# Kernel tuning notes

Measured on AMD Instinct MI355X. Metric: run time of the kernel, lower is better.

## Reference

```python
import jax, jax.numpy as jnp
import numpy as np


def setup_inputs() -> dict:
    key = jax.random.key(0)
    kx, ky, kq, kk, kv = jax.random.split(key, 5)
    B, S, D = 4, 4096, 1024
    scale = 1.0 / np.sqrt(D)
    return {
        "X": jax.random.normal(kx, (B, S, D), dtype=jnp.float32),
        "Y": jax.random.normal(ky, (B, S, D), dtype=jnp.float32),
        "Wq": jax.random.normal(kq, (D, D), dtype=jnp.float32) * scale,
        "Wk": jax.random.normal(kk, (D, D), dtype=jnp.float32) * scale,
        "Wv": jax.random.normal(kv, (D, D), dtype=jnp.float32) * scale,
    }


def reference(X, Y, Wq, Wk, Wv):
    # Single-head windowed cross attention.
    # torch nn.Linear(y) == y @ W.T
    WINDOW = 256
    B, S, D = X.shape
    Q = jnp.einsum("bsd,ed->bse", Y, Wq)
    K = jnp.einsum("bsd,ed->bse", X, Wk)
    V = jnp.einsum("bsd,ed->bse", X, Wv)
    scores = jnp.einsum("bqd,bkd->bqk", Q, K) / jnp.sqrt(jnp.float32(D))
    i = jnp.arange(S)
    band = jnp.abs(i[:, None] - i[None, :]) <= WINDOW  # [S, S]
    NEG = jnp.float32(-1e10)  # matches torch masked_fill value
    scores = jnp.where(band[None, :, :], scores, NEG)
    attn = jax.nn.softmax(scores, axis=-1)
    return jnp.einsum("bqk,bkd->bqd", attn, V)
```

## Files before the change

kernel.cpp:

```cpp
#include <hip/hip_runtime.h>
#include <hip/hip_bf16.h>
#include <stdint.h>

typedef _Float16 half8 __attribute__((ext_vector_type(8)));
typedef float floatx4 __attribute__((ext_vector_type(4)));

#define MFMA16(a, b, c) __builtin_amdgcn_mfma_f32_16x16x32_f16(a, b, c, 0, 0, 0)

__device__ __forceinline__ void async_load16(const void* g, void* l) {
    __builtin_amdgcn_global_load_lds((__attribute__((address_space(1))) void*)(g),
                                     (__attribute__((address_space(3))) void*)(l),
                                     16, 0, 0);
}

#define RAW_BARRIER()  asm volatile("s_barrier" ::: "memory")
#define WAIT_VMCNT(n)  asm volatile("s_waitcnt vmcnt(" #n ")" ::: "memory")
#define WAIT_LGKM0()   asm volatile("s_waitcnt lgkmcnt(0)" ::: "memory")


__global__ __launch_bounds__(256) void cvt_kernel(const float* __restrict__ in,
                                                  _Float16* __restrict__ out,
                                                  int n, float scale) {
    int i = (blockIdx.x * 256 + threadIdx.x) * 8;
    if (i >= n) return;
    float4 v0 = *(const float4*)(in + i);
    float4 v1 = *(const float4*)(in + i + 4);
    half8 h;
    h[0] = (_Float16)(v0.x * scale);
    h[1] = (_Float16)(v0.y * scale);
    h[2] = (_Float16)(v0.z * scale);
    h[3] = (_Float16)(v0.w * scale);
    h[4] = (_Float16)(v1.x * scale);
    h[5] = (_Float16)(v1.y * scale);
    h[6] = (_Float16)(v1.z * scale);
    h[7] = (_Float16)(v1.w * scale);
    *(half8*)(out + i) = h;
}

__global__ __launch_bounds__(512, 2) void gemm_bt(const _Float16* __restrict__ A,
                                                  const _Float16* __restrict__ B,
                                                  _Float16* __restrict__ C,
                                                  int M, int N, int K) {
    __shared__ _Float16 sA[2][2][256 * 32];
    __shared__ _Float16 sB[2][2][256 * 32];
    const int tid  = threadIdx.x;
    const int lane = tid & 63;
    const int w    = tid >> 6;
    const int quad = lane >> 4;
    const int m16  = lane & 15;
    const int mq   = (w >> 2) * 64;
    const int nq   = (w & 3) * 32;

    const int gx = gridDim.x, gy = gridDim.y;
    const int total = gx * gy;
    const int id = blockIdx.y * gx + blockIdx.x;
    const int logical = (id & 7) * (total >> 3) + (id >> 3);
    int bx, by;
    if (gx <= gy) { bx = logical % gx; by = logical / gx; }
    else          { by = logical % gy; bx = logical / gy; }
    const long row0 = (long)by * 256;
    const long col0 = (long)bx * 256;

    floatx4 acc[8][4] = {};

    const int swz = ((tid & 3) ^ ((tid >> 3) & 3)) * 8;
    const _Float16* ga = A + (row0 + (tid >> 2)) * (long)K + swz;
    const _Float16* gb = B + (col0 + (tid >> 2)) * (long)K + swz;
    const int wchunk = w * 1024;

    auto stageA = [&](int tile, int half) {
        const int s = tile & 1;
        char* l0 = (char*)sA[s][0] + half * 8192 + wchunk;
        char* l1 = (char*)sA[s][1] + half * 8192 + wchunk;
        const _Float16* g = ga + (long)tile * 64 + (long)half * 128 * K;
        async_load16(g, l0);
        async_load16(g + 32, l1);
    };
    auto stageB = [&](int tile, int half) {
        const int s = tile & 1;
        char* l0 = (char*)sB[s][0] + half * 8192 + wchunk;
        char* l1 = (char*)sB[s][1] + half * 8192 + wchunk;
        const _Float16* g = gb + (long)tile * 64 + (long)half * 128 * K;
        async_load16(g, l0);
        async_load16(g + 32, l1);
    };

    const int rswz = (m16 >> 1) & 3;
    const int NTt  = K >> 6;

    stageA(0, 0); stageA(0, 1); stageB(0, 0); stageB(0, 1);
    stageA(1, 0); stageB(1, 0);
    WAIT_VMCNT(4);
    RAW_BARRIER();

    for (int U = 0; U < NTt; ++U) {
        const int s = U & 1;
        const int T1 = U + 1, T2 = U + 2;
        half8 af[4][2], bf[2][2];
#pragma unroll
        for (int p = 0; p < 4; ++p) {
            const int mh = p >> 1, nh = p & 1;
            if ((p & 1) == 0) {
#pragma unroll
                for (int mt = 0; mt < 4; mt++)
#pragma unroll
                    for (int j = 0; j < 2; j++)
                        af[mt][j] = *(const half8*)(sA[s][j] +
                            (mh * 128 + mq + mt * 16 + m16) * 32 + (quad ^ rswz) * 8);
            }
#pragma unroll
            for (int nt = 0; nt < 2; nt++)
#pragma unroll
                for (int j = 0; j < 2; j++)
                    bf[nt][j] = *(const half8*)(sB[s][j] +
                        (nh * 128 + nq + nt * 16 + m16) * 32 + (quad ^ rswz) * 8);
            if (p == 0 && T1 < NTt) stageB(T1, 1);
            if (p == 1 && T1 < NTt) stageA(T1, 1);
            if (p == 2 && T2 < NTt) stageA(T2, 0);
            if (p == 3 && T2 < NTt) stageB(T2, 0);
            if (p == 3) {
                if (T2 < NTt) { WAIT_VMCNT(4); }
                else          { WAIT_VMCNT(0); }
            }
            RAW_BARRIER();
            WAIT_LGKM0();
            __builtin_amdgcn_sched_barrier(0);
            __builtin_amdgcn_s_setprio(1);
#pragma unroll
            for (int mt = 0; mt < 4; mt++)
#pragma unroll
                for (int nt = 0; nt < 2; nt++) {
                    acc[mh * 4 + mt][nh * 2 + nt] =
                        MFMA16(af[mt][0], bf[nt][0], acc[mh * 4 + mt][nh * 2 + nt]);
                    acc[mh * 4 + mt][nh * 2 + nt] =
                        MFMA16(af[mt][1], bf[nt][1], acc[mh * 4 + mt][nh * 2 + nt]);
                }
            __builtin_amdgcn_s_setprio(0);
            RAW_BARRIER();
        }
    }

#pragma unroll
    for (int mt = 0; mt < 8; mt++)
#pragma unroll
        for (int nt = 0; nt < 4; nt++)
#pragma unroll
            for (int reg = 0; reg < 4; reg++) {
                long r = row0 + (mt >> 2) * 128 + mq + (mt & 3) * 16 + quad * 4 + reg;
                long c = col0 + (nt >> 1) * 128 + nq + (nt & 1) * 16 + m16;
                C[r * N + c] = (_Float16)acc[mt][nt][reg];
            }
}

__global__ __launch_bounds__(512) void qk_kernel(const _Float16* __restrict__ Qh,
                                                 const _Float16* __restrict__ Kh,
                                                 _Float16* __restrict__ Pg,
                                                 float* __restrict__ invSum) {
    const int S = 4096, D = 1024;
    __shared__ _Float16 sK[2][576 * 32];
    __shared__ _Float16 sQ[2][64 * 32];
    __shared__ float sMax[64][8];
    __shared__ float sSum[64][8];

    const int tid  = threadIdx.x;
    const int lane = tid & 63;
    const int w    = tid >> 6;
    const int quad = lane >> 4;
    const int c16  = lane & 15;
    const int qblk = (blockIdx.x & 7) * 32 + (blockIdx.x >> 3);
    const int b    = qblk >> 6;
    const int q0   = (qblk & 63) << 6;

    int kstart = q0 - 256; if (kstart < 0) kstart = 0;
    int kend   = q0 + 320; if (kend > S) kend = S;
    const int L = kend - kstart;
    const int ntiles = L >> 4;

    const int lrow = lane >> 2;
    const int swz  = ((lane & 3) ^ ((lane >> 3) & 3)) * 8;
    const _Float16* Kbase = Kh + ((long)(b * S + kstart) + lrow) * D + swz;
    const _Float16* Qbase = Qh + ((long)(b * S + q0) + w * 16 + lrow) * D + swz;

    auto stage = [&](int bi, int kc) {
#pragma unroll
        for (int j = 0; j < 5; j++) {
            int g = j * 8 + w;
            if (g < ntiles)
                async_load16(Kbase + (long)g * 16 * D + kc, (char*)sK[bi] + g * 1024);
        }
        if (w < 4)
            async_load16(Qbase + kc, (char*)sQ[bi] + w * 1024);
    };

    const int rswz = ((c16 >> 1) & 3);

    floatx4 acc[4][5] = {};
    stage(0, 0);
    for (int kc = 0; kc < 1024; kc += 32) {
        const int bi = (kc >> 5) & 1;
        __syncthreads();
        if (kc + 32 < 1024) stage(bi ^ 1, kc + 32);
        half8 aQ[4];
#pragma unroll
        for (int mt = 0; mt < 4; mt++)
            aQ[mt] = *(const half8*)(sQ[bi] + (mt * 16 + c16) * 32 + (quad ^ rswz) * 8);
#pragma unroll
        for (int i = 0; i < 5; i++) {
            int t = w + i * 8;
            if (t < ntiles) {
                half8 bK = *(const half8*)(sK[bi] + (t * 16 + c16) * 32 + (quad ^ rswz) * 8);
#pragma unroll
                for (int mt = 0; mt < 4; mt++)
                    acc[mt][i] = MFMA16(aQ[mt], bK, acc[mt][i]);
            }
        }
    }

#pragma unroll
    for (int i = 0; i < 5; i++) {
        int t = w + i * 8;
        if (t < ntiles) {
            int j = kstart + t * 16 + c16;
#pragma unroll
            for (int mt = 0; mt < 4; mt++)
#pragma unroll
                for (int r = 0; r < 4; r++) {
                    int qi = q0 + mt * 16 + quad * 4 + r;
                    int dd = qi - j; dd = dd < 0 ? -dd : dd;
                    if (dd > 256) acc[mt][i][r] = -1e30f;
                }
        }
    }
#pragma unroll
    for (int mt = 0; mt < 4; mt++)
#pragma unroll
        for (int r = 0; r < 4; r++) {
            float m = -1e30f;
#pragma unroll
            for (int i = 0; i < 5; i++)
                if (w + i * 8 < ntiles) m = fmaxf(m, acc[mt][i][r]);
#pragma unroll
            for (int off = 1; off < 16; off <<= 1) m = fmaxf(m, __shfl_xor(m, off, 64));
            if (c16 == 0) sMax[mt * 16 + quad * 4 + r][w] = m;
        }
    __syncthreads();
    if (tid < 64) {
        float fm = sMax[tid][0];
#pragma unroll
        for (int j = 1; j < 8; j++) fm = fmaxf(fm, sMax[tid][j]);
        sMax[tid][0] = fm;
    }
    __syncthreads();
#pragma unroll
    for (int mt = 0; mt < 4; mt++)
#pragma unroll
        for (int r = 0; r < 4; r++) {
            int row = mt * 16 + quad * 4 + r;
            float fm = sMax[row][0];
            float s = 0.f;
#pragma unroll
            for (int i = 0; i < 5; i++) {
                int t = w + i * 8;
                if (t < ntiles) {
                    float e = __expf(acc[mt][i][r] - fm);
                    s += e;
                    Pg[(long)qblk * 36864 + row * 576 + t * 16 + c16] = (_Float16)e;
                }
            }
#pragma unroll
            for (int off = 1; off < 16; off <<= 1) s += __shfl_xor(s, off, 64);
            if (c16 == 0) sSum[row][w] = s;
        }
    __syncthreads();
    if (tid < 64) {
        float t = 0.f;
#pragma unroll
        for (int j = 0; j < 8; j++) t += sSum[tid][j];
        invSum[qblk * 64 + tid] = 1.f / t;
    }
}

__global__ __launch_bounds__(512) void pv_kernel(const _Float16* __restrict__ Pg,
                                                 const float* __restrict__ invSum,
                                                 const _Float16* __restrict__ Vt,
                                                 float* __restrict__ out) {
    const int S = 4096, D = 1024, TOK = 16384;
    __shared__ _Float16 sA[2][64 * 32];
    __shared__ _Float16 sB[2][256 * 32];

    const int tid  = threadIdx.x;
    const int lane = tid & 63;
    const int w    = tid >> 6;
    const int quad = lane >> 4;
    const int c16  = lane & 15;

    const int logical = (blockIdx.x & 7) * 128 + (blockIdx.x >> 3);
    const int qblk = logical >> 2;
    const int n0   = (logical & 3) << 8;
    const int b    = qblk >> 6;
    const int q0   = (qblk & 63) << 6;

    int kstart = q0 - 256; if (kstart < 0) kstart = 0;
    int kend   = q0 + 320; if (kend > S) kend = S;
    const int nsteps = (kend - kstart) >> 5;

    const int lrow = lane >> 2;
    const int swz  = ((lane & 3) ^ ((lane >> 3) & 3)) * 8;
    const _Float16* Abase = Pg + (long)qblk * 36864 + (w * 16 + lrow) * 576 + swz;
    const _Float16* Bbase = Vt + (long)(n0 + lrow) * TOK + b * S + kstart + swz;

    auto stage = [&](int bi, int kc) {
        if (w < 4)
            async_load16(Abase + kc, (char*)sA[bi] + w * 1024);
#pragma unroll
        for (int j = 0; j < 2; j++) {
            int g = j * 8 + w;
            async_load16(Bbase + (long)g * 16 * TOK + kc, (char*)sB[bi] + g * 1024);
        }
    };

    const int wm = (w >> 2) * 32;
    const int wn = (w & 3) * 64;
    const int rswz = ((c16 >> 1) & 3);
    floatx4 acc[2][4] = {};

    stage(0, 0);
    for (int s = 0; s < nsteps; s++) {
        const int bi = s & 1;
        __syncthreads();
        if (s + 1 < nsteps) stage(bi ^ 1, (s + 1) * 32);
        half8 aA[2], bB[4];
#pragma unroll
        for (int mt = 0; mt < 2; mt++)
            aA[mt] = *(const half8*)(sA[bi] + (wm + mt * 16 + c16) * 32 + (quad ^ rswz) * 8);
#pragma unroll
        for (int nt = 0; nt < 4; nt++)
            bB[nt] = *(const half8*)(sB[bi] + (wn + nt * 16 + c16) * 32 + (quad ^ rswz) * 8);
#pragma unroll
        for (int mt = 0; mt < 2; mt++)
#pragma unroll
            for (int nt = 0; nt < 4; nt++)
                acc[mt][nt] = MFMA16(aA[mt], bB[nt], acc[mt][nt]);
    }

    const float* isB = invSum + qblk * 64;
#pragma unroll
    for (int mt = 0; mt < 2; mt++)
#pragma unroll
        for (int nt = 0; nt < 4; nt++)
#pragma unroll
            for (int reg = 0; reg < 4; reg++) {
                int row = wm + mt * 16 + quad * 4 + reg;
                int col = n0 + wn + nt * 16 + c16;
                out[(long)(b * S + q0 + row) * D + col] = acc[mt][nt][reg] * isB[row];
            }
}

extern "C" void kernel_launch(void* const* d_in, const int* in_sizes, int n_in,
                              void* d_out, int out_size, void* d_ws, size_t ws_size,
                              hipStream_t stream) {
    const float* X  = (const float*)d_in[0];
    const float* Y  = (const float*)d_in[1];
    const float* Wq = (const float*)d_in[2];
    const float* Wk = (const float*)d_in[3];
    const float* Wv = (const float*)d_in[4];
    float* out = (float*)d_out;

    const long NTOK = 16384, D = 1024;
    char* p = (char*)d_ws;
    _Float16* Xh  = (_Float16*)p; p += NTOK * D * 2;
    _Float16* Yh  = (_Float16*)p; p += NTOK * D * 2;
    _Float16* Wqh = (_Float16*)p; p += D * D * 2;
    _Float16* Wkh = (_Float16*)p; p += D * D * 2;
    _Float16* Wvh = (_Float16*)p; p += D * D * 2;
    _Float16* Qh  = (_Float16*)p; p += NTOK * D * 2;
    _Float16* Vt  = (_Float16*)p; p += NTOK * D * 2;
    _Float16* Kh  = Yh;
    _Float16* Pg  = Xh;
    float* invSum = (float*)(Xh + 256l * 64 * 576);

    const int nT = (int)(NTOK * D);
    const int nW = (int)(D * D);
    cvt_kernel<<<nT / 2048, 256, 0, stream>>>(X, Xh, nT, 1.f);
    cvt_kernel<<<nT / 2048, 256, 0, stream>>>(Y, Yh, nT, 1.f);
    cvt_kernel<<<nW / 2048, 256, 0, stream>>>(Wq, Wqh, nW, 0.03125f);
    cvt_kernel<<<nW / 2048, 256, 0, stream>>>(Wk, Wkh, nW, 1.f);
    cvt_kernel<<<nW / 2048, 256, 0, stream>>>(Wv, Wvh, nW, 1.f);

    gemm_bt<<<dim3(1024 / 256, 16384 / 256), 512, 0, stream>>>(Yh, Wqh, Qh, 16384, 1024, 1024);
    gemm_bt<<<dim3(1024 / 256, 16384 / 256), 512, 0, stream>>>(Xh, Wkh, Kh, 16384, 1024, 1024);
    gemm_bt<<<dim3(16384 / 256, 1024 / 256), 512, 0, stream>>>(Wvh, Xh, Vt, 1024, 16384, 1024);

    qk_kernel<<<dim3(256), 512, 0, stream>>>(Qh, Kh, Pg, invSum);
    pv_kernel<<<dim3(4 * 256), 512, 0, stream>>>(Pg, invSum, Vt, out);
}
```

Before: 377.3 us.

## Deepen async-load prefetch with explicit vmcnt waits and uniform tile loads

Both the score and PV kernels now issue two stages of async global-to-LDS loads up front and wait with per-wave vmcnt counts and raw barriers instead of __syncthreads. The next-next stage is issued after compute finishes, so loads overlap a full iteration of MFMA work. In the score kernel the per-tile bounds checks are replaced by a fixed wave-dependent tile count, so vmcnt stays uniform. Padded tiles are masked to a large negative value and not written out. Edge blocks may load padding rows past the valid key range, and correctness now relies on the hand-counted vmcnt values.

New measurement: 377.4 us. About the same (+0.0%).

```diff
diff --git a/kernel.cpp b/kernel.cpp
--- a/kernel.cpp
+++ b/kernel.cpp
@@ -173,8 +173,7 @@
 
     int kstart = q0 - 256; if (kstart < 0) kstart = 0;
     int kend   = q0 + 320; if (kend > S) kend = S;
-    const int L = kend - kstart;
-    const int ntiles = L >> 4;
+    const int ntReal = (kend - kstart) >> 4;
 
     const int lrow = lane >> 2;
     const int swz  = ((lane & 3) ^ ((lane >> 3) & 3)) * 8;
@@ -184,9 +183,10 @@
     auto stage = [&](int bi, int kc) {
 #pragma unroll
         for (int j = 0; j < 5; j++) {
-            int g = j * 8 + w;
-            if (g < ntiles)
+            if (j < 4 || w < 4) {
+                int g = j * 8 + w;
                 async_load16(Kbase + (long)g * 16 * D + kc, (char*)sK[bi] + g * 1024);
+            }
         }
         if (w < 4)
             async_load16(Qbase + kc, (char*)sQ[bi] + w * 1024);
@@ -196,38 +196,47 @@
 
     floatx4 acc[4][5] = {};
     stage(0, 0);
+    stage(1, 32);
     for (int kc = 0; kc < 1024; kc += 32) {
         const int bi = (kc >> 5) & 1;
-        __syncthreads();
-        if (kc + 32 < 1024) stage(bi ^ 1, kc + 32);
+        if (kc + 32 < 1024) {
+            if (w < 4) { WAIT_VMCNT(6); } else { WAIT_VMCNT(4); }
+        } else {
+            WAIT_VMCNT(0);
+        }
+        RAW_BARRIER();
         half8 aQ[4];
 #pragma unroll
         for (int mt = 0; mt < 4; mt++)
             aQ[mt] = *(const half8*)(sQ[bi] + (mt * 16 + c16) * 32 + (quad ^ rswz) * 8);
 #pragma unroll
         for (int i = 0; i < 5; i++) {
-            int t = w + i * 8;
-            if (t < ntiles) {
+            if (i < 4 || w < 4) {
+                int t = w + i * 8;
                 half8 bK = *(const half8*)(sK[bi] + (t * 16 + c16) * 32 + (quad ^ rswz) * 8);
 #pragma unroll
                 for (int mt = 0; mt < 4; mt++)
                     acc[mt][i] = MFMA16(aQ[mt], bK, acc[mt][i]);
             }
         }
+        WAIT_LGKM0();
+        RAW_BARRIER();
+        if (kc + 64 < 1024) stage(bi, kc + 64);
     }
 
 #pragma unroll
     for (int i = 0; i < 5; i++) {
-        int t = w + i * 8;
-        if (t < ntiles) {
+        if (i < 4 || w < 4) {
+            int t = w + i * 8;
             int j = kstart + t * 16 + c16;
+            bool pad = (t >= ntReal);
 #pragma unroll
             for (int mt = 0; mt < 4; mt++)
 #pragma unroll
                 for (int r = 0; r < 4; r++) {
                     int qi = q0 + mt * 16 + quad * 4 + r;
                     int dd = qi - j; dd = dd < 0 ? -dd : dd;
-                    if (dd > 256) acc[mt][i][r] = -1e30f;
+                    if (dd > 256 || pad) acc[mt][i][r] = -1e30f;
                 }
         }
     }
@@ -238,7 +247,7 @@
             float m = -1e30f;
 #pragma unroll
             for (int i = 0; i < 5; i++)
-                if (w + i * 8 < ntiles) m = fmaxf(m, acc[mt][i][r]);
+                if (i < 4 || w < 4) m = fmaxf(m, acc[mt][i][r]);
 #pragma unroll
             for (int off = 1; off < 16; off <<= 1) m = fmaxf(m, __shfl_xor(m, off, 64));
             if (c16 == 0) sMax[mt * 16 + quad * 4 + r][w] = m;
@@ -260,11 +269,12 @@
             float s = 0.f;
 #pragma unroll
             for (int i = 0; i < 5; i++) {
-                int t = w + i * 8;
-                if (t < ntiles) {
+                if (i < 4 || w < 4) {
+                    int t = w + i * 8;
                     float e = __expf(acc[mt][i][r] - fm);
                     s += e;
-                    Pg[(long)qblk * 36864 + row * 576 + t * 16 + c16] = (_Float16)e;
+                    if (t < ntReal)
+                        Pg[(long)qblk * 36864 + row * 576 + t * 16 + c16] = (_Float16)e;
                 }
             }
 #pragma unroll
@@ -325,10 +335,15 @@
     floatx4 acc[2][4] = {};
 
     stage(0, 0);
+    stage(1, 32);
     for (int s = 0; s < nsteps; s++) {
         const int bi = s & 1;
-        __syncthreads();
-        if (s + 1 < nsteps) stage(bi ^ 1, (s + 1) * 32);
+        if (s + 1 < nsteps) {
+            if (w < 4) { WAIT_VMCNT(3); } else { WAIT_VMCNT(2); }
+        } else {
+            WAIT_VMCNT(0);
+        }
+        RAW_BARRIER();
         half8 aA[2], bB[4];
 #pragma unroll
         for (int mt = 0; mt < 2; mt++)
@@ -341,6 +356,9 @@
 #pragma unroll
             for (int nt = 0; nt < 4; nt++)
                 acc[mt][nt] = MFMA16(aA[mt], bB[nt], acc[mt][nt]);
+        WAIT_LGKM0();
+        RAW_BARRIER();
+        if (s + 2 < nsteps) stage(bi, (s + 2) * 32);
     }
 
     const float* isB = invSum + qblk * 64;
```
